# Performance work log

Hardware: AMD Instinct MI355X
Metric: run time of the kernel (lower is better)

The kernel has to match this reference:

```python
import jax, jax.numpy as jnp
import numpy as np

RADIUS = 0.05
HMIN = -0.02
HMAXES = (0.01, 0.02, 0.03, 0.04)
NSAMPLE = 64
BN_EPS = 1e-5


def _group(d_rot, hmax):
    # d_rot: (B,S,N,3) seed-relative coords rotated into the gripper frame (d @ R)
    # Cylinder query: approach axis is x; keep first NSAMPLE points with
    # y^2+z^2 < r^2 and hmin < x < hmax; pad with first hit (0 if no hit),
    # matching the CUDA cylinder_query kernel semantics.
    N = d_rot.shape[2]
    h = d_rot[..., 0]
    r2 = d_rot[..., 1] ** 2 + d_rot[..., 2] ** 2
    mask = (r2 < RADIUS * RADIUS) & (h > HMIN) & (h < hmax)
    key = jnp.where(mask, jnp.arange(N, dtype=jnp.int32), N)
    neg_top, _ = jax.lax.top_k(-key, NSAMPLE)   # ascending keys = first hits in point order
    idx = -neg_top                               # (B,S,k); == N where slot is invalid
    first = idx[..., :1]
    idx = jnp.where(idx < N, idx, jnp.where(first < N, first, 0))
    return jnp.take_along_axis(d_rot, idx[..., None], axis=2)  # (B,S,k,3)


def _mlp_layer(x, w, b, g, be, m, v):
    # 1x1 Conv2d + BatchNorm (eval-mode, running stats) + ReLU, as in pt_utils.SharedMLP
    x = jnp.einsum('bcpn,oc->bopn', x, w) + b[None, :, None, None]
    scale = g / jnp.sqrt(v + BN_EPS)
    x = (x - m[None, :, None, None]) * scale[None, :, None, None] + be[None, :, None, None]
    return jax.nn.relu(x)


def _forward(seed_xyz, pointcloud, vp_rot, params):
    B, S, _ = seed_xyz.shape
    D = len(HMAXES)
    d = pointcloud[:, None, :, :] - seed_xyz[:, :, None, :]          # (B,S,N,3)
    d_rot = jnp.einsum('bsnc,bscd->bsnd', d, vp_rot)                 # rotate into gripper frame
    groups = jnp.stack([_group(d_rot, h) for h in HMAXES], axis=2)   # (B,S,D,k,3)
    x = groups.transpose(0, 4, 1, 2, 3).reshape(B, 3, S * D, NSAMPLE)  # (B,3,S*D,k)
    for (w, b, g, be, m, v) in params:
        x = _mlp_layer(x, w, b, g, be, m, v)
    x = x.max(axis=-1)                                               # max-pool over nsample
    return x.reshape(B, -1, S, D)                                    # (B,256,S,D)


def setup_inputs() -> dict:
    key = jax.random.key(0)
    ks = jax.random.split(key, 8)
    B, S, N = 2, 1024, 16384
    inp = {
        'seed_xyz': jax.random.uniform(ks[0], (B, S, 3), jnp.float32),
        'pointcloud': jax.random.uniform(ks[1], (B, N, 3), jnp.float32),
        'vp_rot': jax.random.normal(ks[2], (B, S, 3, 3), jnp.float32),
    }
    dims = [3, 64, 128, 256]
    for i in range(3):
        cin, cout = dims[i], dims[i + 1]
        k1, k2, k3, k4, k5, k6 = jax.random.split(ks[3 + i], 6)
        inp[f'w{i+1}'] = jax.random.normal(k1, (cout, cin), jnp.float32) * 0.05
        inp[f'b{i+1}'] = jax.random.normal(k2, (cout,), jnp.float32) * 0.01
        inp[f'g{i+1}'] = 1.0 + 0.1 * jax.random.normal(k3, (cout,), jnp.float32)
        inp[f'be{i+1}'] = jax.random.normal(k4, (cout,), jnp.float32) * 0.01
        inp[f'm{i+1}'] = jax.random.normal(k5, (cout,), jnp.float32) * 0.01
        inp[f'v{i+1}'] = jax.random.uniform(k6, (cout,), jnp.float32, 0.5, 1.5)
    return inp


def reference(seed_xyz, pointcloud, vp_rot,
              w1, b1, g1, be1, m1, v1,
              w2, b2, g2, be2, m2, v2,
              w3, b3, g3, be3, m3, v3):
    params = [(w1, b1, g1, be1, m1, v1),
              (w2, b2, g2, be2, m2, v2),
              (w3, b3, g3, be3, m3, v3)]
    return _forward(seed_xyz, pointcloud, vp_rot, params)
```

## Files before the change

kernel.cpp:

```cpp
#include <hip/hip_runtime.h>
#include <hip/hip_bf16.h>
#include <cstdint>
#include <cstddef>

#define NSAMP  64
#define NPT    16384
#define NLVL   4
#define NCHUNK 8
#define CHSZ   (NPT / NCHUNK)

typedef __attribute__((ext_vector_type(8))) short  short8;
typedef __attribute__((ext_vector_type(4))) float  floatx4;
typedef __attribute__((ext_vector_type(4))) unsigned int uintx4;
typedef __attribute__((ext_vector_type(2))) unsigned int uintx2;

__device__ __forceinline__ unsigned short f2bf(float x) {
    union { float f; unsigned int u; } c; c.f = x;
    unsigned int r = (c.u + 0x7fffu + ((c.u >> 16) & 1u)) >> 16;
    return (unsigned short)r;
}
__device__ __forceinline__ unsigned int f2bf2(float a, float b) {
    __hip_bfloat162 t = __float22bfloat162_rn(make_float2(a, b));
    union { __hip_bfloat162 h; unsigned int u; } c; c.h = t;
    return c.u;
}

__global__ __launch_bounds__(256) void prep_kernel(
    const float* __restrict__ w1, const float* __restrict__ b1, const float* __restrict__ g1,
    const float* __restrict__ be1, const float* __restrict__ m1, const float* __restrict__ v1,
    const float* __restrict__ w2, const float* __restrict__ b2, const float* __restrict__ g2,
    const float* __restrict__ be2, const float* __restrict__ m2, const float* __restrict__ v2,
    const float* __restrict__ w3, const float* __restrict__ b3, const float* __restrict__ g3,
    const float* __restrict__ be3, const float* __restrict__ m3, const float* __restrict__ v3,
    float* __restrict__ w1f, float* __restrict__ fb1,
    unsigned short* __restrict__ w2b, float* __restrict__ fb2,
    unsigned short* __restrict__ w3b, float* __restrict__ fb3)
{
    const int t  = blockIdx.x * 256 + threadIdx.x;
    const int nt = gridDim.x * 256;
    const float eps = 1e-5f;
    for (int i = t; i < 64 * 3; i += nt)    w1f[i] = w1[i] * (g1[i / 3] / sqrtf(v1[i / 3] + eps));
    for (int i = t; i < 64; i += nt)        fb1[i] = (b1[i] - m1[i]) * (g1[i] / sqrtf(v1[i] + eps)) + be1[i];
    for (int i = t; i < 128 * 64; i += nt)  w2b[i] = f2bf(w2[i] * (g2[i / 64] / sqrtf(v2[i / 64] + eps)));
    for (int i = t; i < 128; i += nt)       fb2[i] = (b2[i] - m2[i]) * (g2[i] / sqrtf(v2[i] + eps)) + be2[i];
    for (int i = t; i < 256 * 128; i += nt) w3b[i] = f2bf(w3[i] * (g3[i / 128] / sqrtf(v3[i / 128] + eps)));
    for (int i = t; i < 256; i += nt)       fb3[i] = (b3[i] - m3[i]) * (g3[i] / sqrtf(v3[i] + eps)) + be3[i];
}

__global__ __launch_bounds__(512) void scan_kernel(
    const float* __restrict__ seedp, const float* __restrict__ pc,
    const float* __restrict__ rot, unsigned short* __restrict__ buf,
    int* __restrict__ cnts)
{
    __shared__ float ch[CHSZ * 3];
    const int tid  = threadIdx.x;
    const int lane = tid & 63;
    const int w    = tid >> 6;
    const int sg   = blockIdx.x >> 3;
    const int c    = blockIdx.x & 7;
    const int g    = sg * 8 + w;
    const int b    = g >> 10;

    {
        const float4* src = (const float4*)(pc + ((size_t)b * NPT + c * CHSZ) * 3);
        float4* dst = (float4*)ch;
        dst[tid]        = src[tid];
        dst[tid + 512]  = src[tid + 512];
        dst[tid + 1024] = src[tid + 1024];
    }
    __syncthreads();

    const float* sd = seedp + (size_t)g * 3;
    const float sx = sd[0], sy = sd[1], sz = sd[2];
    const float* R = rot + (size_t)g * 9;
    const float r00 = R[0], r01 = R[1], r02 = R[2];
    const float r10 = R[3], r11 = R[4], r12 = R[5];
    const float r20 = R[6], r21 = R[7], r22 = R[8];
    const float nc0 = -(sx * r00 + sy * r10 + sz * r20);
    const float nc1 = -(sx * r01 + sy * r11 + sz * r21);
    const float nc2 = -(sx * r02 + sy * r12 + sz * r22);

    unsigned short* bufg = buf + (size_t)g * (NLVL * NCHUNK * 64);
    int cnt0 = 0, cnt1 = 0, cnt2 = 0, cnt3 = 0;
    const unsigned long long lm = (1ull << lane) - 1ull;

    for (int bt = 0; bt < 4; ++bt) {
        float pxv[8], pyv[8], pzv[8];
        #pragma unroll
        for (int j = 0; j < 8; ++j) {
            const int pl = (bt * 8 + j) * 64 + lane;
            pxv[j] = ch[pl * 3];
            pyv[j] = ch[pl * 3 + 1];
            pzv[j] = ch[pl * 3 + 2];
        }
        #pragma unroll
        for (int j = 0; j < 8; ++j) {
            const float h = fmaf(pxv[j], r00, fmaf(pyv[j], r10, fmaf(pzv[j], r20, nc0)));
            const float u = fmaf(pxv[j], r01, fmaf(pyv[j], r11, fmaf(pzv[j], r21, nc1)));
            const float v = fmaf(pxv[j], r02, fmaf(pyv[j], r12, fmaf(pzv[j], r22, nc2)));
            const float r2 = fmaf(u, u, v * v);
            const bool base = (r2 < 0.0025f) && (h > -0.02f) && (h < 0.04f);

            const unsigned long long bal3 = __ballot(base);
            if (bal3 == 0ull) continue;

            const unsigned short pidx = (unsigned short)(c * CHSZ + (bt * 8 + j) * 64 + lane);
            #pragma unroll
            for (int l = 0; l < NLVL; ++l) {
                unsigned long long bal; bool m;
                if (l == 3) { m = base; bal = bal3; }
                else {
                    const float hm = (l == 0) ? 0.01f : (l == 1) ? 0.02f : 0.03f;
                    m = base && (h < hm);
                    bal = __ballot(m);
                }
                int& cnt = (l == 0) ? cnt0 : (l == 1) ? cnt1 : (l == 2) ? cnt2 : cnt3;
                if (m) {
                    const int pos = cnt + (int)__popcll(bal & lm);
                    if (pos < 64) bufg[(l * NCHUNK + c) * 64 + pos] = pidx;
                }
                cnt += (int)__popcll(bal);
            }
        }
        if (cnt0 >= NSAMP) break;
    }

    if (lane == 0) {
        int* cg = cnts + (size_t)g * (NLVL * NCHUNK);
        cg[0 * NCHUNK + c] = cnt0;
        cg[1 * NCHUNK + c] = cnt1;
        cg[2 * NCHUNK + c] = cnt2;
        cg[3 * NCHUNK + c] = cnt3;
    }
}

__global__ __launch_bounds__(256) void gather_kernel(
    const float* __restrict__ seedp, const float* __restrict__ pc,
    const float* __restrict__ rot,
    const unsigned short* __restrict__ buf, const int* __restrict__ cnts,
    float* __restrict__ gx)
{
    const int n = threadIdx.x & 63;
    const int W = blockIdx.x * 4 + (threadIdx.x >> 6);
    const int g = W >> 2, l = W & 3;
    const int b = g >> 10;

    const int* cg = cnts + (size_t)g * (NLVL * NCHUNK) + l * NCHUNK;
    const unsigned short* bl = buf + (size_t)g * (NLVL * NCHUNK * 64) + l * (NCHUNK * 64);
    int idx = -1, acc = 0, firstIdx = -1;
    #pragma unroll
    for (int c = 0; c < NCHUNK; ++c) {
        const int cn = min(cg[c], 64);
        if (cn > 0 && firstIdx < 0) firstIdx = (int)bl[c * 64];
        if (n >= acc && n < acc + cn) idx = (int)bl[c * 64 + (n - acc)];
        acc += cn;
    }
    if (idx < 0) idx = (firstIdx >= 0) ? firstIdx : 0;

    const float* sd = seedp + (size_t)g * 3;
    const float* R  = rot   + (size_t)g * 9;
    const float* pp = pc + ((size_t)b * NPT + idx) * 3;
    const float dx = pp[0] - sd[0], dy = pp[1] - sd[1], dz = pp[2] - sd[2];

    float* o = gx + (size_t)W * 192;
    o[n]       = dx * R[0] + dy * R[3] + dz * R[6];
    o[64 + n]  = dx * R[1] + dy * R[4] + dz * R[7];
    o[128 + n] = dx * R[2] + dy * R[5] + dz * R[8];
}

__global__ __launch_bounds__(256) void mlp_kernel(
    const float* __restrict__ gx,
    const float* __restrict__ w1f, const float* __restrict__ fb1,
    const unsigned short* __restrict__ w2b, const float* __restrict__ fb2,
    const unsigned short* __restrict__ w3b, const float* __restrict__ fb3,
    float* __restrict__ out)
{
    __shared__ unsigned short h1t[4096];
    __shared__ unsigned short h2t[8192];

    const int tid = threadIdx.x;
    const int n      = tid & 63;
    const int w      = tid >> 6;
    const int lane15 = tid & 15;
    const int quad   = (tid & 63) >> 4;

    short8 wa3[4][4];
    float  wb3[4];
    #pragma unroll
    for (int mt = 0; mt < 4; ++mt) {
        const int m0 = (w * 4 + mt) * 16;
        #pragma unroll
        for (int k0 = 0; k0 < 4; ++k0)
            wa3[mt][k0] = *(const short8*)&w3b[(m0 + lane15) * 128 + k0 * 32 + quad * 8];
        wb3[mt] = fb3[m0 + lane15];
    }

    short8 a20[2], a21[2]; floatx4 b2v[2];
    #pragma unroll
    for (int mi = 0; mi < 2; ++mi) {
        const int m0 = (w * 2 + mi) * 16;
        a20[mi] = *(const short8*)&w2b[(m0 + lane15) * 64 + quad * 8];
        a21[mi] = *(const short8*)&w2b[(m0 + lane15) * 64 + 32 + quad * 8];
        b2v[mi] = *(const floatx4*)&fb2[m0 + quad * 4];
    }

    {
        const float* xb = gx + (size_t)(blockIdx.x * 4) * 192;
        const float x0 = xb[n], x1 = xb[64 + n], x2 = xb[128 + n];
        unsigned int p[8];
        #pragma unroll
        for (int j = 0; j < 8; ++j) {
            const int o0 = __builtin_amdgcn_readfirstlane(w * 16 + 2 * j);
            const float a0 = fb1[o0]     + w1f[o0*3]*x0   + w1f[o0*3+1]*x1 + w1f[o0*3+2]*x2;
            const float a1 = fb1[o0 + 1] + w1f[o0*3+3]*x0 + w1f[o0*3+4]*x1 + w1f[o0*3+5]*x2;
            p[j] = f2bf2(fmaxf(a0, 0.f), fmaxf(a1, 0.f));
        }
        *(uintx4*)&h1t[(((w * 2)    ) * 64 + n) * 8] = (uintx4){p[0], p[1], p[2], p[3]};
        *(uintx4*)&h1t[(((w * 2) + 1) * 64 + n) * 8] = (uintx4){p[4], p[5], p[6], p[7]};
    }

    for (int it = 0; it < 4; ++it) {
        const int gp = blockIdx.x * 4 + it;
        const int g = gp >> 2, l = gp & 3;
        const int b = g >> 10, s = g & 1023;

        __syncthreads();

        {
            short8 bfr[4][2];
            #pragma unroll
            for (int nt = 0; nt < 4; ++nt)
                #pragma unroll
                for (int k0 = 0; k0 < 2; ++k0)
                    bfr[nt][k0] = *(const short8*)&h1t[((k0 * 4 + quad) * 64 + nt * 16 + lane15) * 8];

            #pragma unroll
            for (int mi = 0; mi < 2; ++mi) {
                const int m0 = (w * 2 + mi) * 16;
                #pragma unroll
                for (int nt = 0; nt < 4; ++nt) {
                    floatx4 acc = b2v[mi];
                    acc = __builtin_amdgcn_mfma_f32_16x16x32_bf16(a20[mi], bfr[nt][0], acc, 0, 0, 0);
                    acc = __builtin_amdgcn_mfma_f32_16x16x32_bf16(a21[mi], bfr[nt][1], acc, 0, 0, 0);
                    const int n2 = nt * 16 + lane15;
                    const unsigned int q0 = f2bf2(fmaxf(acc[0], 0.f), fmaxf(acc[1], 0.f));
                    const unsigned int q1 = f2bf2(fmaxf(acc[2], 0.f), fmaxf(acc[3], 0.f));
                    const int kb = (m0 >> 3) + (quad >> 1);
                    *(uintx2*)&h2t[(kb * 64 + n2) * 8 + (quad & 1) * 4] = (uintx2){q0, q1};
                }
            }
        }
        __syncthreads();

        short8 bfr3[4][4];
        #pragma unroll
        for (int nt = 0; nt < 4; ++nt)
            #pragma unroll
            for (int k0 = 0; k0 < 4; ++k0)
                bfr3[nt][k0] = *(const short8*)&h2t[((k0 * 4 + quad) * 64 + nt * 16 + lane15) * 8];

        if (it < 3) {
            const float* xb = gx + (size_t)(gp + 1) * 192;
            const float x0 = xb[n], x1 = xb[64 + n], x2 = xb[128 + n];
            unsigned int p[8];
            #pragma unroll
            for (int j = 0; j < 8; ++j) {
                const int o0 = __builtin_amdgcn_readfirstlane(w * 16 + 2 * j);
                const float a0 = fb1[o0]     + w1f[o0*3]*x0   + w1f[o0*3+1]*x1 + w1f[o0*3+2]*x2;
                const float a1 = fb1[o0 + 1] + w1f[o0*3+3]*x0 + w1f[o0*3+4]*x1 + w1f[o0*3+5]*x2;
                p[j] = f2bf2(fmaxf(a0, 0.f), fmaxf(a1, 0.f));
            }
            *(uintx4*)&h1t[(((w * 2)    ) * 64 + n) * 8] = (uintx4){p[0], p[1], p[2], p[3]};
            *(uintx4*)&h1t[(((w * 2) + 1) * 64 + n) * 8] = (uintx4){p[4], p[5], p[6], p[7]};
        }

        #pragma unroll
        for (int mt = 0; mt < 4; ++mt) {
            const int m0 = (w * 4 + mt) * 16;
            floatx4 acc[4];
            #pragma unroll
            for (int nt = 0; nt < 4; ++nt) acc[nt] = (floatx4){0.f, 0.f, 0.f, 0.f};
            #pragma unroll
            for (int k0 = 0; k0 < 4; ++k0)
                #pragma unroll
                for (int nt = 0; nt < 4; ++nt)
                    acc[nt] = __builtin_amdgcn_mfma_f32_16x16x32_bf16(bfr3[nt][k0], wa3[mt][k0], acc[nt], 0, 0, 0);

            float t0 = fmaxf(fmaxf(acc[0][0], acc[0][1]), fmaxf(acc[0][2], acc[0][3]));
            float t1 = fmaxf(fmaxf(acc[1][0], acc[1][1]), fmaxf(acc[1][2], acc[1][3]));
            float t2 = fmaxf(fmaxf(acc[2][0], acc[2][1]), fmaxf(acc[2][2], acc[2][3]));
            float t3 = fmaxf(fmaxf(acc[3][0], acc[3][1]), fmaxf(acc[3][2], acc[3][3]));
            float t  = fmaxf(fmaxf(t0, t1), fmaxf(t2, t3));
            t = fmaxf(t, __shfl_xor(t, 16));
            t = fmaxf(t, __shfl_xor(t, 32));
            if (quad == 0) {
                const int o = m0 + lane15;
                out[(((size_t)b * 256 + o) * 1024 + s) * 4 + l] = fmaxf(t + wb3[mt], 0.f);
            }
        }
    }
}

extern "C" void kernel_launch(void* const* d_in, const int* in_sizes, int n_in,
                              void* d_out, int out_size, void* d_ws, size_t ws_size,
                              hipStream_t stream) {
    const float* seed = (const float*)d_in[0];
    const float* pc   = (const float*)d_in[1];
    const float* rot  = (const float*)d_in[2];
    const float* w1 = (const float*)d_in[3];
    const float* b1 = (const float*)d_in[4];
    const float* g1 = (const float*)d_in[5];
    const float* be1 = (const float*)d_in[6];
    const float* m1 = (const float*)d_in[7];
    const float* v1 = (const float*)d_in[8];
    const float* w2 = (const float*)d_in[9];
    const float* b2 = (const float*)d_in[10];
    const float* g2 = (const float*)d_in[11];
    const float* be2 = (const float*)d_in[12];
    const float* m2 = (const float*)d_in[13];
    const float* v2 = (const float*)d_in[14];
    const float* w3 = (const float*)d_in[15];
    const float* b3 = (const float*)d_in[16];
    const float* g3 = (const float*)d_in[17];
    const float* be3 = (const float*)d_in[18];
    const float* m3 = (const float*)d_in[19];
    const float* v3 = (const float*)d_in[20];

    float* w1f = (float*)d_ws;
    float* fb1 = w1f + 192;
    float* fb2 = fb1 + 64;
    float* fb3 = fb2 + 128;
    unsigned short* w2b = (unsigned short*)(fb3 + 256);
    unsigned short* w3b = w2b + 8192;
    unsigned short* buf = w3b + 32768;
    int* cnts = (int*)(buf + 4194304);
    float* gx = (float*)(cnts + 65536);

    prep_kernel<<<64, 256, 0, stream>>>(w1, b1, g1, be1, m1, v1,
                                        w2, b2, g2, be2, m2, v2,
                                        w3, b3, g3, be3, m3, v3,
                                        w1f, fb1, w2b, fb2, w3b, fb3);
    scan_kernel<<<2048, 512, 0, stream>>>(seed, pc, rot, buf, cnts);
    gather_kernel<<<2048, 256, 0, stream>>>(seed, pc, rot, buf, cnts, gx);
    mlp_kernel<<<2048, 256, 0, stream>>>(gx, w1f, fb1, w2b, fb2, w3b, fb3,
                                         (float*)d_out);
}
```

Measured before the change: 183.3 us.

## Fuse cylinder scan and gather into one per-seed kernel with double-buffered chunks

Merges the scan and gather kernels so that each wavefront handles one seed and walks all eight point-cloud chunks in sequence. Chunks are staged through a double-buffered LDS tile that is prefetched via registers. Hit indices are kept in LDS lists instead of a global buffer with per-chunk counts, which removes a launch and the intermediate global traffic. The cost is far less parallelism: 512 blocks of 4 waves replace 2048 blocks of 8 waves. Each block also re-reads the whole point cloud for only 4 seeds, and the early exit rarely triggers, so nearly every chunk is still scanned.

```diff
diff --git a/kernel.cpp b/kernel.cpp
--- a/kernel.cpp
+++ b/kernel.cpp
@@ -47,28 +47,20 @@
     for (int i = t; i < 256; i += nt)       fb3[i] = (b3[i] - m3[i]) * (g3[i] / sqrtf(v3[i] + eps)) + be3[i];
 }
 
-__global__ __launch_bounds__(512) void scan_kernel(
+__global__ __launch_bounds__(256) void scan2_kernel(
     const float* __restrict__ seedp, const float* __restrict__ pc,
-    const float* __restrict__ rot, unsigned short* __restrict__ buf,
-    int* __restrict__ cnts)
+    const float* __restrict__ rot, float* __restrict__ gx)
 {
-    __shared__ float ch[CHSZ * 3];
+    __shared__ float ch[2][CHSZ * 3];
+    __shared__ unsigned short lists[4][NLVL][64];
+
     const int tid  = threadIdx.x;
     const int lane = tid & 63;
     const int w    = tid >> 6;
-    const int sg   = blockIdx.x >> 3;
-    const int c    = blockIdx.x & 7;
-    const int g    = sg * 8 + w;
+    const int g    = blockIdx.x * 4 + w;
     const int b    = g >> 10;
 
-    {
-        const float4* src = (const float4*)(pc + ((size_t)b * NPT + c * CHSZ) * 3);
-        float4* dst = (float4*)ch;
-        dst[tid]        = src[tid];
-        dst[tid + 512]  = src[tid + 512];
-        dst[tid + 1024] = src[tid + 1024];
-    }
-    __syncthreads();
+    const float* pcb = pc + (size_t)b * NPT * 3;
 
     const float* sd = seedp + (size_t)g * 3;
     const float sx = sd[0], sy = sd[1], sz = sd[2];
@@ -80,92 +72,92 @@
     const float nc1 = -(sx * r01 + sy * r11 + sz * r21);
     const float nc2 = -(sx * r02 + sy * r12 + sz * r22);
 
-    unsigned short* bufg = buf + (size_t)g * (NLVL * NCHUNK * 64);
     int cnt0 = 0, cnt1 = 0, cnt2 = 0, cnt3 = 0;
     const unsigned long long lm = (1ull << lane) - 1ull;
 
-    for (int bt = 0; bt < 4; ++bt) {
-        float pxv[8], pyv[8], pzv[8];
-        #pragma unroll
-        for (int j = 0; j < 8; ++j) {
-            const int pl = (bt * 8 + j) * 64 + lane;
-            pxv[j] = ch[pl * 3];
-            pyv[j] = ch[pl * 3 + 1];
-            pzv[j] = ch[pl * 3 + 2];
-        }
-        #pragma unroll
-        for (int j = 0; j < 8; ++j) {
-            const float h = fmaf(pxv[j], r00, fmaf(pyv[j], r10, fmaf(pzv[j], r20, nc0)));
-            const float u = fmaf(pxv[j], r01, fmaf(pyv[j], r11, fmaf(pzv[j], r21, nc1)));
-            const float v = fmaf(pxv[j], r02, fmaf(pyv[j], r12, fmaf(pzv[j], r22, nc2)));
-            const float r2 = fmaf(u, u, v * v);
-            const bool base = (r2 < 0.0025f) && (h > -0.02f) && (h < 0.04f);
-
-            const unsigned long long bal3 = __ballot(base);
-            if (bal3 == 0ull) continue;
-
-            const unsigned short pidx = (unsigned short)(c * CHSZ + (bt * 8 + j) * 64 + lane);
-            #pragma unroll
-            for (int l = 0; l < NLVL; ++l) {
-                unsigned long long bal; bool m;
-                if (l == 3) { m = base; bal = bal3; }
-                else {
-                    const float hm = (l == 0) ? 0.01f : (l == 1) ? 0.02f : 0.03f;
-                    m = base && (h < hm);
-                    bal = __ballot(m);
+    float4 st[6];
+    {
+        const float4* src = (const float4*)pcb;
+        #pragma unroll
+        for (int k = 0; k < 6; ++k) st[k] = src[tid + 256 * k];
+    }
+
+    for (int c = 0; c < NCHUNK; ++c) {
+        {
+            float4* dst = (float4*)ch[c & 1];
+            #pragma unroll
+            for (int k = 0; k < 6; ++k) dst[tid + 256 * k] = st[k];
+        }
+        if (c < NCHUNK - 1) {
+            const float4* src = (const float4*)(pcb + (size_t)(c + 1) * CHSZ * 3);
+            #pragma unroll
+            for (int k = 0; k < 6; ++k) st[k] = src[tid + 256 * k];
+        }
+        __syncthreads();
+
+        const float* chb = ch[c & 1];
+        if (cnt0 < NSAMP) {
+            for (int bt = 0; bt < 4; ++bt) {
+                float pxv[8], pyv[8], pzv[8];
+                #pragma unroll
+                for (int j = 0; j < 8; ++j) {
+                    const int pl = (bt * 8 + j) * 64 + lane;
+                    pxv[j] = chb[pl * 3];
+                    pyv[j] = chb[pl * 3 + 1];
+                    pzv[j] = chb[pl * 3 + 2];
                 }
-                int& cnt = (l == 0) ? cnt0 : (l == 1) ? cnt1 : (l == 2) ? cnt2 : cnt3;
-                if (m) {
-                    const int pos = cnt + (int)__popcll(bal & lm);
-                    if (pos < 64) bufg[(l * NCHUNK + c) * 64 + pos] = pidx;
+                #pragma unroll
+                for (int j = 0; j < 8; ++j) {
+                    const float h = fmaf(pxv[j], r00, fmaf(pyv[j], r10, fmaf(pzv[j], r20, nc0)));
+                    const float u = fmaf(pxv[j], r01, fmaf(pyv[j], r11, fmaf(pzv[j], r21, nc1)));
+                    const float v = fmaf(pxv[j], r02, fmaf(pyv[j], r12, fmaf(pzv[j], r22, nc2)));
+                    const float r2 = fmaf(u, u, v * v);
+                    const bool base = (r2 < 0.0025f) && (h > -0.02f) && (h < 0.04f);
+
+                    const unsigned long long bal3 = __ballot(base);
+                    if (bal3 == 0ull) continue;
+
+                    const unsigned short pidx = (unsigned short)(c * CHSZ + (bt * 8 + j) * 64 + lane);
+                    #pragma unroll
+                    for (int l = 0; l < NLVL; ++l) {
+                        unsigned long long bal; bool m;
+                        if (l == 3) { m = base; bal = bal3; }
+                        else {
+                            const float hm = (l == 0) ? 0.01f : (l == 1) ? 0.02f : 0.03f;
+                            m = base && (h < hm);
+                            bal = __ballot(m);
+                        }
+                        int& cnt = (l == 0) ? cnt0 : (l == 1) ? cnt1 : (l == 2) ? cnt2 : cnt3;
+                        if (m) {
+                            const int pos = cnt + (int)__popcll(bal & lm);
+                            if (pos < 64) lists[w][l][pos] = pidx;
+                        }
+                        cnt += (int)__popcll(bal);
+                    }
                 }
-                cnt += (int)__popcll(bal);
+                if (cnt0 >= NSAMP) break;
             }
         }
-        if (cnt0 >= NSAMP) break;
-    }
-
-    if (lane == 0) {
-        int* cg = cnts + (size_t)g * (NLVL * NCHUNK);
-        cg[0 * NCHUNK + c] = cnt0;
-        cg[1 * NCHUNK + c] = cnt1;
-        cg[2 * NCHUNK + c] = cnt2;
-        cg[3 * NCHUNK + c] = cnt3;
-    }
-}
-
-__global__ __launch_bounds__(256) void gather_kernel(
-    const float* __restrict__ seedp, const float* __restrict__ pc,
-    const float* __restrict__ rot,
-    const unsigned short* __restrict__ buf, const int* __restrict__ cnts,
-    float* __restrict__ gx)
-{
-    const int n = threadIdx.x & 63;
-    const int W = blockIdx.x * 4 + (threadIdx.x >> 6);
-    const int g = W >> 2, l = W & 3;
-    const int b = g >> 10;
-
-    const int* cg = cnts + (size_t)g * (NLVL * NCHUNK) + l * NCHUNK;
-    const unsigned short* bl = buf + (size_t)g * (NLVL * NCHUNK * 64) + l * (NCHUNK * 64);
-    int idx = -1, acc = 0, firstIdx = -1;
+    }
+
+    __syncthreads();
+
     #pragma unroll
-    for (int c = 0; c < NCHUNK; ++c) {
-        const int cn = min(cg[c], 64);
-        if (cn > 0 && firstIdx < 0) firstIdx = (int)bl[c * 64];
-        if (n >= acc && n < acc + cn) idx = (int)bl[c * 64 + (n - acc)];
-        acc += cn;
-    }
-    if (idx < 0) idx = (firstIdx >= 0) ? firstIdx : 0;
-
-    const float* sd = seedp + (size_t)g * 3;
-    const float* R  = rot   + (size_t)g * 9;
-    const float* pp = pc + ((size_t)b * NPT + idx) * 3;
-    const float dx = pp[0] - sd[0], dy = pp[1] - sd[1], dz = pp[2] - sd[2];
-
-    float* o = gx + (size_t)W * 192;
-    o[n]       = dx * R[0] + dy * R[3] + dz * R[6];
-    o[64 + n]  = dx * R[1] + dy * R[4] + dz * R[7];
-    o[128 + n] = dx * R[2] + dy * R[5] + dz * R[8];
+    for (int l = 0; l < NLVL; ++l) {
+        const int cnt = (l == 0) ? cnt0 : (l == 1) ? cnt1 : (l == 2) ? cnt2 : cnt3;
+        const int kn = min(cnt, 64);
+        int idx;
+        if (lane < kn)      idx = (int)lists[w][l][lane];
+        else if (kn > 0)    idx = (int)lists[w][l][0];
+        else                idx = 0;
+
+        const float* pp = pcb + (size_t)idx * 3;
+        const float dx = pp[0] - sx, dy = pp[1] - sy, dz = pp[2] - sz;
+        float* o = gx + (size_t)(g * NLVL + l) * 192;
+        o[lane]       = dx * r00 + dy * r10 + dz * r20;
+        o[64 + lane]  = dx * r01 + dy * r11 + dz * r21;
+        o[128 + lane] = dx * r02 + dy * r12 + dz * r22;
+    }
 }
 
 __global__ __launch_bounds__(256) void mlp_kernel(
@@ -332,16 +324,13 @@
     float* fb3 = fb2 + 128;
     unsigned short* w2b = (unsigned short*)(fb3 + 256);
     unsigned short* w3b = w2b + 8192;
-    unsigned short* buf = w3b + 32768;
-    int* cnts = (int*)(buf + 4194304);
-    float* gx = (float*)(cnts + 65536);
+    float* gx = (float*)(w3b + 32768);
 
     prep_kernel<<<64, 256, 0, stream>>>(w1, b1, g1, be1, m1, v1,
                                         w2, b2, g2, be2, m2, v2,
                                         w3, b3, g3, be3, m3, v3,
                                         w1f, fb1, w2b, fb2, w3b, fb3);
-    scan_kernel<<<2048, 512, 0, stream>>>(seed, pc, rot, buf, cnts);
-    gather_kernel<<<2048, 256, 0, stream>>>(seed, pc, rot, buf, cnts, gx);
+    scan2_kernel<<<512, 256, 0, stream>>>(seed, pc, rot, gx);
     mlp_kernel<<<2048, 256, 0, stream>>>(gx, w1f, fb1, w2b, fb2, w3b, fb3,
                                          (float*)d_out);
 }
```

Result: slower. 219.9 us (+20.0%).

## Restructure MLP kernel to one wavefront per group with register-built layer-1 fragments

Applied to the files above, without the earlier changes.

Replaces the 4-wave, 4-group-per-block MLP kernel with a single-wavefront kernel that handles one group per block over 8192 blocks. Layer 1 is computed directly into MFMA B-fragments in registers, and its weights and bias are packed into float4 so each pair of channels needs fewer loads. This removes the h1 shared buffer and all __syncthreads. In exchange, every wave now reloads all layer-2 and layer-3 weights from global/L2 per group instead of keeping them resident across four groups, and layer-1 arithmetic is repeated per lane quad.

```diff
diff --git a/kernel.cpp b/kernel.cpp
--- a/kernel.cpp
+++ b/kernel.cpp
@@ -32,15 +32,20 @@
     const float* __restrict__ be2, const float* __restrict__ m2, const float* __restrict__ v2,
     const float* __restrict__ w3, const float* __restrict__ b3, const float* __restrict__ g3,
     const float* __restrict__ be3, const float* __restrict__ m3, const float* __restrict__ v3,
-    float* __restrict__ w1f, float* __restrict__ fb1,
+    float* __restrict__ w1p,
     unsigned short* __restrict__ w2b, float* __restrict__ fb2,
     unsigned short* __restrict__ w3b, float* __restrict__ fb3)
 {
     const int t  = blockIdx.x * 256 + threadIdx.x;
     const int nt = gridDim.x * 256;
     const float eps = 1e-5f;
-    for (int i = t; i < 64 * 3; i += nt)    w1f[i] = w1[i] * (g1[i / 3] / sqrtf(v1[i / 3] + eps));
-    for (int i = t; i < 64; i += nt)        fb1[i] = (b1[i] - m1[i]) * (g1[i] / sqrtf(v1[i] + eps)) + be1[i];
+    for (int i = t; i < 64; i += nt) {
+        const float sc = g1[i] / sqrtf(v1[i] + eps);
+        w1p[i * 4 + 0] = w1[i * 3 + 0] * sc;
+        w1p[i * 4 + 1] = w1[i * 3 + 1] * sc;
+        w1p[i * 4 + 2] = w1[i * 3 + 2] * sc;
+        w1p[i * 4 + 3] = (b1[i] - m1[i]) * sc + be1[i];
+    }
     for (int i = t; i < 128 * 64; i += nt)  w2b[i] = f2bf(w2[i] * (g2[i / 64] / sqrtf(v2[i / 64] + eps)));
     for (int i = t; i < 128; i += nt)       fb2[i] = (b2[i] - m2[i]) * (g2[i] / sqrtf(v2[i] + eps)) + be2[i];
     for (int i = t; i < 256 * 128; i += nt) w3b[i] = f2bf(w3[i] * (g3[i / 128] / sqrtf(v3[i / 128] + eps)));
@@ -168,135 +173,101 @@
     o[128 + n] = dx * R[2] + dy * R[5] + dz * R[8];
 }
 
-__global__ __launch_bounds__(256) void mlp_kernel(
+__global__ __launch_bounds__(64) void mlp2_kernel(
     const float* __restrict__ gx,
-    const float* __restrict__ w1f, const float* __restrict__ fb1,
+    const float* __restrict__ w1p,
     const unsigned short* __restrict__ w2b, const float* __restrict__ fb2,
     const unsigned short* __restrict__ w3b, const float* __restrict__ fb3,
     float* __restrict__ out)
 {
-    __shared__ unsigned short h1t[4096];
-    __shared__ unsigned short h2t[8192];
-
-    const int tid = threadIdx.x;
-    const int n      = tid & 63;
-    const int w      = tid >> 6;
-    const int lane15 = tid & 15;
-    const int quad   = (tid & 63) >> 4;
-
-    short8 wa3[4][4];
-    float  wb3[4];
-    #pragma unroll
-    for (int mt = 0; mt < 4; ++mt) {
-        const int m0 = (w * 4 + mt) * 16;
+    __shared__ unsigned short h2[8192];
+
+    const int lane   = threadIdx.x;
+    const int lane15 = lane & 15;
+    const int quad   = lane >> 4;
+
+    const int gp = blockIdx.x;
+    const int g = gp >> 2, l = gp & 3;
+    const int b = g >> 10, s = g & 1023;
+
+    const float* xb = gx + (size_t)gp * 192;
+    float x0v[4], x1v[4], x2v[4];
+    #pragma unroll
+    for (int nt = 0; nt < 4; ++nt) {
+        const int n = nt * 16 + lane15;
+        x0v[nt] = xb[n]; x1v[nt] = xb[64 + n]; x2v[nt] = xb[128 + n];
+    }
+
+    union { unsigned int u[4][2][4]; short8 s8[4][2]; } B1;
+    #pragma unroll
+    for (int k0 = 0; k0 < 2; ++k0) {
+        #pragma unroll
+        for (int j = 0; j < 4; ++j) {
+            const int ch = k0 * 32 + quad * 8 + 2 * j;
+            const floatx4 wa = *(const floatx4*)&w1p[ch * 4];
+            const floatx4 wb = *(const floatx4*)&w1p[ch * 4 + 4];
+            #pragma unroll
+            for (int nt = 0; nt < 4; ++nt) {
+                const float a0 = wa[3] + wa[0]*x0v[nt] + wa[1]*x1v[nt] + wa[2]*x2v[nt];
+                const float a1 = wb[3] + wb[0]*x0v[nt] + wb[1]*x1v[nt] + wb[2]*x2v[nt];
+                B1.u[nt][k0][j] = f2bf2(fmaxf(a0, 0.f), fmaxf(a1, 0.f));
+            }
+        }
+    }
+
+    #pragma unroll
+    for (int mi = 0; mi < 8; ++mi) {
+        const short8 a0v = *(const short8*)&w2b[(mi * 16 + lane15) * 64 + quad * 8];
+        const short8 a1v = *(const short8*)&w2b[(mi * 16 + lane15) * 64 + 32 + quad * 8];
+        const floatx4 bias = *(const floatx4*)&fb2[mi * 16 + quad * 4];
+        const int kb = mi * 2 + (quad >> 1);
+        #pragma unroll
+        for (int nt = 0; nt < 4; ++nt) {
+            floatx4 acc = bias;
+            acc = __builtin_amdgcn_mfma_f32_16x16x32_bf16(a0v, B1.s8[nt][0], acc, 0, 0, 0);
+            acc = __builtin_amdgcn_mfma_f32_16x16x32_bf16(a1v, B1.s8[nt][1], acc, 0, 0, 0);
+            const unsigned int q0 = f2bf2(fmaxf(acc[0], 0.f), fmaxf(acc[1], 0.f));
+            const unsigned int q1 = f2bf2(fmaxf(acc[2], 0.f), fmaxf(acc[3], 0.f));
+            const int n2 = nt * 16 + lane15;
+            *(uintx2*)&h2[(kb * 64 + n2) * 8 + (quad & 1) * 4] = (uintx2){q0, q1};
+        }
+    }
+
+    short8 bfr3[4][4];
+    #pragma unroll
+    for (int nt = 0; nt < 4; ++nt)
         #pragma unroll
         for (int k0 = 0; k0 < 4; ++k0)
-            wa3[mt][k0] = *(const short8*)&w3b[(m0 + lane15) * 128 + k0 * 32 + quad * 8];
-        wb3[mt] = fb3[m0 + lane15];
-    }
-
-    short8 a20[2], a21[2]; floatx4 b2v[2];
-    #pragma unroll
-    for (int mi = 0; mi < 2; ++mi) {
-        const int m0 = (w * 2 + mi) * 16;
-        a20[mi] = *(const short8*)&w2b[(m0 + lane15) * 64 + quad * 8];
-        a21[mi] = *(const short8*)&w2b[(m0 + lane15) * 64 + 32 + quad * 8];
-        b2v[mi] = *(const floatx4*)&fb2[m0 + quad * 4];
-    }
-
-    {
-        const float* xb = gx + (size_t)(blockIdx.x * 4) * 192;
-        const float x0 = xb[n], x1 = xb[64 + n], x2 = xb[128 + n];
-        unsigned int p[8];
-        #pragma unroll
-        for (int j = 0; j < 8; ++j) {
-            const int o0 = __builtin_amdgcn_readfirstlane(w * 16 + 2 * j);
-            const float a0 = fb1[o0]     + w1f[o0*3]*x0   + w1f[o0*3+1]*x1 + w1f[o0*3+2]*x2;
-            const float a1 = fb1[o0 + 1] + w1f[o0*3+3]*x0 + w1f[o0*3+4]*x1 + w1f[o0*3+5]*x2;
-            p[j] = f2bf2(fmaxf(a0, 0.f), fmaxf(a1, 0.f));
-        }
-        *(uintx4*)&h1t[(((w * 2)    ) * 64 + n) * 8] = (uintx4){p[0], p[1], p[2], p[3]};
-        *(uintx4*)&h1t[(((w * 2) + 1) * 64 + n) * 8] = (uintx4){p[4], p[5], p[6], p[7]};
-    }
-
-    for (int it = 0; it < 4; ++it) {
-        const int gp = blockIdx.x * 4 + it;
-        const int g = gp >> 2, l = gp & 3;
-        const int b = g >> 10, s = g & 1023;
-
-        __syncthreads();
-
-        {
-            short8 bfr[4][2];
+            bfr3[nt][k0] = *(const short8*)&h2[((k0 * 4 + quad) * 64 + nt * 16 + lane15) * 8];
+
+    #pragma unroll
+    for (int mt = 0; mt < 16; ++mt) {
+        const int m0 = mt * 16;
+        short8 wk[4];
+        #pragma unroll
+        for (int k0 = 0; k0 < 4; ++k0)
+            wk[k0] = *(const short8*)&w3b[(m0 + lane15) * 128 + k0 * 32 + quad * 8];
+        const float bias3 = fb3[m0 + lane15];
+
+        floatx4 acc[4];
+        #pragma unroll
+        for (int nt = 0; nt < 4; ++nt) acc[nt] = (floatx4){0.f, 0.f, 0.f, 0.f};
+        #pragma unroll
+        for (int k0 = 0; k0 < 4; ++k0)
             #pragma unroll
             for (int nt = 0; nt < 4; ++nt)
-                #pragma unroll
-                for (int k0 = 0; k0 < 2; ++k0)
-                    bfr[nt][k0] = *(const short8*)&h1t[((k0 * 4 + quad) * 64 + nt * 16 + lane15) * 8];
-
-            #pragma unroll
-            for (int mi = 0; mi < 2; ++mi) {
-                const int m0 = (w * 2 + mi) * 16;
-                #pragma unroll
-                for (int nt = 0; nt < 4; ++nt) {
-                    floatx4 acc = b2v[mi];
-                    acc = __builtin_amdgcn_mfma_f32_16x16x32_bf16(a20[mi], bfr[nt][0], acc, 0, 0, 0);
-                    acc = __builtin_amdgcn_mfma_f32_16x16x32_bf16(a21[mi], bfr[nt][1], acc, 0, 0, 0);
-                    const int n2 = nt * 16 + lane15;
-                    const unsigned int q0 = f2bf2(fmaxf(acc[0], 0.f), fmaxf(acc[1], 0.f));
-                    const unsigned int q1 = f2bf2(fmaxf(acc[2], 0.f), fmaxf(acc[3], 0.f));
-                    const int kb = (m0 >> 3) + (quad >> 1);
-                    *(uintx2*)&h2t[(kb * 64 + n2) * 8 + (quad & 1) * 4] = (uintx2){q0, q1};
-                }
-            }
-        }
-        __syncthreads();
-
-        short8 bfr3[4][4];
-        #pragma unroll
-        for (int nt = 0; nt < 4; ++nt)
-            #pragma unroll
-            for (int k0 = 0; k0 < 4; ++k0)
-                bfr3[nt][k0] = *(const short8*)&h2t[((k0 * 4 + quad) * 64 + nt * 16 + lane15) * 8];
-
-        if (it < 3) {
-            const float* xb = gx + (size_t)(gp + 1) * 192;
-            const float x0 = xb[n], x1 = xb[64 + n], x2 = xb[128 + n];
-            unsigned int p[8];
-            #pragma unroll
-            for (int j = 0; j < 8; ++j) {
-                const int o0 = __builtin_amdgcn_readfirstlane(w * 16 + 2 * j);
-                const float a0 = fb1[o0]     + w1f[o0*3]*x0   + w1f[o0*3+1]*x1 + w1f[o0*3+2]*x2;
-                const float a1 = fb1[o0 + 1] + w1f[o0*3+3]*x0 + w1f[o0*3+4]*x1 + w1f[o0*3+5]*x2;
-                p[j] = f2bf2(fmaxf(a0, 0.f), fmaxf(a1, 0.f));
-            }
-            *(uintx4*)&h1t[(((w * 2)    ) * 64 + n) * 8] = (uintx4){p[0], p[1], p[2], p[3]};
-            *(uintx4*)&h1t[(((w * 2) + 1) * 64 + n) * 8] = (uintx4){p[4], p[5], p[6], p[7]};
-        }
-
-        #pragma unroll
-        for (int mt = 0; mt < 4; ++mt) {
-            const int m0 = (w * 4 + mt) * 16;
-            floatx4 acc[4];
-            #pragma unroll
-            for (int nt = 0; nt < 4; ++nt) acc[nt] = (floatx4){0.f, 0.f, 0.f, 0.f};
-            #pragma unroll
-            for (int k0 = 0; k0 < 4; ++k0)
-                #pragma unroll
-                for (int nt = 0; nt < 4; ++nt)
-                    acc[nt] = __builtin_amdgcn_mfma_f32_16x16x32_bf16(bfr3[nt][k0], wa3[mt][k0], acc[nt], 0, 0, 0);
-
-            float t0 = fmaxf(fmaxf(acc[0][0], acc[0][1]), fmaxf(acc[0][2], acc[0][3]));
-            float t1 = fmaxf(fmaxf(acc[1][0], acc[1][1]), fmaxf(acc[1][2], acc[1][3]));
-            float t2 = fmaxf(fmaxf(acc[2][0], acc[2][1]), fmaxf(acc[2][2], acc[2][3]));
-            float t3 = fmaxf(fmaxf(acc[3][0], acc[3][1]), fmaxf(acc[3][2], acc[3][3]));
-            float t  = fmaxf(fmaxf(t0, t1), fmaxf(t2, t3));
-            t = fmaxf(t, __shfl_xor(t, 16));
-            t = fmaxf(t, __shfl_xor(t, 32));
-            if (quad == 0) {
-                const int o = m0 + lane15;
-                out[(((size_t)b * 256 + o) * 1024 + s) * 4 + l] = fmaxf(t + wb3[mt], 0.f);
-            }
+                acc[nt] = __builtin_amdgcn_mfma_f32_16x16x32_bf16(bfr3[nt][k0], wk[k0], acc[nt], 0, 0, 0);
+
+        float t0 = fmaxf(fmaxf(acc[0][0], acc[0][1]), fmaxf(acc[0][2], acc[0][3]));
+        float t1 = fmaxf(fmaxf(acc[1][0], acc[1][1]), fmaxf(acc[1][2], acc[1][3]));
+        float t2 = fmaxf(fmaxf(acc[2][0], acc[2][1]), fmaxf(acc[2][2], acc[2][3]));
+        float t3 = fmaxf(fmaxf(acc[3][0], acc[3][1]), fmaxf(acc[3][2], acc[3][3]));
+        float t  = fmaxf(fmaxf(t0, t1), fmaxf(t2, t3));
+        t = fmaxf(t, __shfl_xor(t, 16));
+        t = fmaxf(t, __shfl_xor(t, 32));
+        if (quad == 0) {
+            const int o = m0 + lane15;
+            out[(((size_t)b * 256 + o) * 1024 + s) * 4 + l] = fmaxf(t + bias3, 0.f);
         }
     }
 }
@@ -326,9 +297,8 @@
     const float* m3 = (const float*)d_in[19];
     const float* v3 = (const float*)d_in[20];
 
-    float* w1f = (float*)d_ws;
-    float* fb1 = w1f + 192;
-    float* fb2 = fb1 + 64;
+    float* w1p = (float*)d_ws;
+    float* fb2 = w1p + 256;
     float* fb3 = fb2 + 128;
     unsigned short* w2b = (unsigned short*)(fb3 + 256);
     unsigned short* w3b = w2b + 8192;
@@ -339,9 +309,9 @@
     prep_kernel<<<64, 256, 0, stream>>>(w1, b1, g1, be1, m1, v1,
                                         w2, b2, g2, be2, m2, v2,
                                         w3, b3, g3, be3, m3, v3,
-                                        w1f, fb1, w2b, fb2, w3b, fb3);
+                                        w1p, w2b, fb2, w3b, fb3);
     scan_kernel<<<2048, 512, 0, stream>>>(seed, pc, rot, buf, cnts);
     gather_kernel<<<2048, 256, 0, stream>>>(seed, pc, rot, buf, cnts, gx);
-    mlp_kernel<<<2048, 256, 0, stream>>>(gx, w1f, fb1, w2b, fb2, w3b, fb3,
+    mlp2_kernel<<<8192, 64, 0, stream>>>(gx, w1p, w2b, fb2, w3b, fb3,
                                          (float*)d_out);
 }
```

Result: slower. 211.8 us (+15.5%).
